# Kernel optimization log

Hardware: AMD Instinct MI355X
Metric: run time of the kernel (lower is better)

Reference implementation:

```python
import jax, jax.numpy as jnp
import numpy as np
from jax import lax

FEAT_STRIDE = 16
SCALES = (8, 16, 32)
RATIOS = (0.5, 1.0, 2.0)
PRE_NMS = 6000
POST_NMS = 300
NMS_THRESH = 0.7
MIN_SIZE = 16.0


def _base_anchors():
    base = 16.0
    cx = cy = base / 2.0
    anchors = []
    for r in RATIOS:
        for s in SCALES:
            h = base * s * np.sqrt(r)
            w = base * s * np.sqrt(1.0 / r)
            anchors.append([cx - w / 2, cy - h / 2, cx + w / 2, cy + h / 2])
    return np.asarray(anchors, np.float32)  # [A,4] (x1,y1,x2,y2)


def _shifted_anchors(h, w):
    base = _base_anchors()
    sy = np.arange(h, dtype=np.float32) * FEAT_STRIDE
    sx = np.arange(w, dtype=np.float32) * FEAT_STRIDE
    yy, xx = np.meshgrid(sy, sx, indexing='ij')  # h-major then w, matching NHWC permute
    shifts = np.stack([xx, yy, xx, yy], axis=-1).reshape(-1, 1, 4)
    return (shifts + base[None]).reshape(-1, 4).astype(np.float32)  # [h*w*A,4]


def _conv(x, w, b, pad):
    y = lax.conv_general_dilated(x, w, (1, 1), [(pad, pad), (pad, pad)],
                                 dimension_numbers=('NCHW', 'OIHW', 'NCHW'))
    return y + b[None, :, None, None]


def _iou(box, boxes):
    lt = jnp.maximum(box[:2], boxes[:, :2])
    rb = jnp.minimum(box[2:], boxes[:, 2:])
    wh = jnp.maximum(rb - lt, 0.0)
    inter = wh[:, 0] * wh[:, 1]
    a1 = (box[2] - box[0]) * (box[3] - box[1])
    a2 = (boxes[:, 2] - boxes[:, 0]) * (boxes[:, 3] - boxes[:, 1])
    return inter / (a1 + a2 - inter + 1e-9)


def _nms_proposals(boxes, scores):
    # boxes [K,4], scores [K] -> [POST_NMS,4]
    ws = boxes[:, 2] - boxes[:, 0]
    hs = boxes[:, 3] - boxes[:, 1]
    scores = jnp.where((ws >= MIN_SIZE) & (hs >= MIN_SIZE), scores, -jnp.inf)
    top_s, idx = lax.top_k(scores, PRE_NMS)
    b = boxes[idx]

    def body(i, st):
        keep, s = st
        j = jnp.argmax(s).astype(jnp.int32)
        keep = keep.at[i].set(j)
        sup = _iou(b[j], b) >= NMS_THRESH  # suppresses j itself too (iou=1)
        s = jnp.where(sup, -jnp.inf, s)
        return keep, s

    keep, _ = lax.fori_loop(0, POST_NMS, body,
                            (jnp.zeros((POST_NMS,), jnp.int32), top_s))
    return b[keep]


def setup_inputs() -> dict:
    key = jax.random.key(0)
    ks = jax.random.split(key, 5)
    n, c, h, w = 8, 512, 50, 64
    A = len(SCALES) * len(RATIOS)
    x = jax.random.normal(ks[0], (n, c, h, w), jnp.float32)
    w1 = jax.random.normal(ks[1], (512, 512, 3, 3), jnp.float32) * 0.02
    b1 = jnp.zeros((512,), jnp.float32)
    w_cls = jax.random.normal(ks[2], (A * 2, 512, 1, 1), jnp.float32) * 0.02
    b_cls = jnp.zeros((A * 2,), jnp.float32)
    w_bbox = jax.random.normal(ks[3], (A * 4, 512, 1, 1), jnp.float32) * 0.005
    b_bbox = jnp.zeros((A * 4,), jnp.float32)
    return {'x': x, 'w1': w1, 'b1': b1, 'w_cls': w_cls, 'b_cls': b_cls,
            'w_bbox': w_bbox, 'b_bbox': b_bbox}


def reference(x, w1, b1, w_cls, b_cls, w_bbox, b_bbox):
    n, _, h, w = x.shape
    A = len(SCALES) * len(RATIOS)
    img_h, img_w = h * FEAT_STRIDE, w * FEAT_STRIDE
    anchors = jnp.asarray(_shifted_anchors(h, w))  # [h*w*A,4]

    feat = jax.nn.relu(_conv(x, w1, b1, 1))
    cls = _conv(feat, w_cls, b_cls, 0).transpose(0, 2, 3, 1).reshape(n, h, w, A, 2)
    fg = jax.nn.softmax(cls, axis=-1)[..., 1].reshape(n, -1)  # [n, h*w*A]
    deltas = _conv(feat, w_bbox, b_bbox, 0).transpose(0, 2, 3, 1).reshape(n, -1, 4)

    # decode deltas against anchors
    aw = anchors[:, 2] - anchors[:, 0]
    ah = anchors[:, 3] - anchors[:, 1]
    acx = anchors[:, 0] + 0.5 * aw
    acy = anchors[:, 1] + 0.5 * ah
    cx = deltas[..., 0] * aw + acx
    cy = deltas[..., 1] * ah + acy
    pw = jnp.exp(deltas[..., 2]) * aw
    ph = jnp.exp(deltas[..., 3]) * ah
    boxes = jnp.stack([cx - 0.5 * pw, cy - 0.5 * ph,
                       cx + 0.5 * pw, cy + 0.5 * ph], axis=-1)  # [n,K,4]
    hi = jnp.asarray([img_w, img_h, img_w, img_h], jnp.float32)
    boxes = jnp.clip(boxes, 0.0, hi)

    rois = jax.vmap(_nms_proposals)(boxes, fg)  # [n,POST_NMS,4]
    roi_indices = jnp.repeat(jnp.arange(n, dtype=jnp.int32), POST_NMS)
    return rois.reshape(-1, 4), roi_indices
```

## Files before the change

kernel.cpp:

```cpp
#include <hip/hip_runtime.h>
#include <math.h>

#define NIMG 8
#define CIN  512
#define HF   50
#define WF   64
#define HW   3200
#define NA   9
#define KPER 28800
#define PRE  6000
#define POST 300

#define WHT_ELEMS  32768

#define NW    94
#define NCAP  6016
#define NTRI  4465

#define XTROWS 52
#define XTCOLS 66
#define XT_ELEMS ((size_t)NIMG * XTROWS * XTCOLS * CIN)
#define XT_BYTES (XT_ELEMS * 2)

#define WPK_ELEMS ((size_t)2 * 4 * 9 * 16 * 4096)
#define WPK_HALF  (4 * 9 * 16 * 4096)

#define SCALE_X 256.0f
#define SCALE_W 16384.0f
#define INV_SCALE (1.0f / 4194304.0f)

#define PB_XT   1600
#define PB_HALO 64
#define PB_WPK  288
#define PB_PH   16
#define PB_TOT  (PB_XT + PB_HALO + PB_WPK + PB_PH)

#define HALO_VPI 14848
#define HALO_TOT (NIMG * HALO_VPI)

typedef _Float16 f16x8 __attribute__((ext_vector_type(8)));
typedef float f32x4  __attribute__((ext_vector_type(4)));
typedef unsigned short u16x8 __attribute__((ext_vector_type(8)));
typedef unsigned long long u64;

__constant__ float BASEA[9][4] = {
  {-82.509667991878083f, -37.254833995939042f,  98.509667991878083f,  53.254833995939042f},
  {-173.01933598375617f, -82.509667991878083f, 189.01933598375617f,   98.509667991878083f},
  {-354.03867196751233f, -173.01933598375617f, 370.03867196751233f,  189.01933598375617f},
  { -56.0f,  -56.0f,  72.0f,  72.0f},
  {-120.0f, -120.0f, 136.0f, 136.0f},
  {-248.0f, -248.0f, 264.0f, 264.0f},
  {-37.254833995939042f, -82.509667991878083f,  53.254833995939042f,  98.509667991878083f},
  {-82.509667991878083f, -173.01933598375617f,  98.509667991878083f, 189.01933598375617f},
  {-173.01933598375617f, -354.03867196751233f, 189.01933598375617f,  370.03867196751233f},
};

__device__ __forceinline__ unsigned int ordf(float f) {
  unsigned int u = __float_as_uint(f);
  return (u & 0x80000000u) ? ~u : (u | 0x80000000u);
}

__device__ __forceinline__ unsigned short f2h(float f) {
  union { _Float16 h; unsigned short u; } cv;
  cv.h = (_Float16)f;
  return cv.u;
}
__device__ __forceinline__ float h2f(unsigned short u) {
  union { _Float16 h; unsigned short u; } cv;
  cv.u = u;
  return (float)cv.h;
}

__global__ __launch_bounds__(256) void k_prep_all(
    const float4* __restrict__ x4,
    const float* __restrict__ w1,
    const float* __restrict__ wc, const float* __restrict__ bc,
    const float* __restrict__ wb, const float* __restrict__ bb,
    unsigned short* __restrict__ xh, unsigned short* __restrict__ xl,
    unsigned short* __restrict__ wpk,
    float* __restrict__ WHT2, float* __restrict__ bh) {
  __shared__ float tile[128][65];
  const int blk = blockIdx.x;
  const int t = threadIdx.x;

  if (blk < PB_XT) {
    const int cic = blk & 3;
    const int rest = blk >> 2;
    const int hrow = rest % 50;
    const int n = rest / 50;
#pragma unroll
    for (int jj = 0; jj < 8; ++jj) {
      const int e = t + 256 * jj;
      const int row = e >> 4, c4 = e & 15;
      const float4 v = x4[(((size_t)(n * CIN + cic * 128 + row) * HF + hrow) << 4) + c4];
      tile[row][c4 * 4 + 0] = v.x;
      tile[row][c4 * 4 + 1] = v.y;
      tile[row][c4 * 4 + 2] = v.z;
      tile[row][c4 * 4 + 3] = v.w;
    }
    __syncthreads();
#pragma unroll
    for (int jj = 0; jj < 4; ++jj) {
      const int e = t + 256 * jj;
      const int w = e >> 4, c8 = e & 15;
      const size_t base = ((size_t)((n * XTROWS + (hrow + 1)) * XTCOLS) + (w + 1)) * CIN
                          + cic * 128 + c8 * 8;
      u16x8 hv, lv;
#pragma unroll
      for (int u = 0; u < 8; ++u) {
        const float g = tile[c8 * 8 + u][w] * SCALE_X;
        const unsigned short hh = f2h(g);
        hv[u] = (short)hh;
        lv[u] = (short)f2h(g - h2f(hh));
      }
      *reinterpret_cast<u16x8*>(xh + base) = hv;
      *reinterpret_cast<u16x8*>(xl + base) = lv;
    }
  } else if (blk < PB_XT + PB_HALO) {
    const u16x8 z = {0, 0, 0, 0, 0, 0, 0, 0};
    const int tid = (blk - PB_XT) * 256 + t;
    for (int v = tid; v < HALO_TOT; v += PB_HALO * 256) {
      const int n = v / HALO_VPI;
      const int r = v - n * HALO_VPI;
      int row, col, v8;
      if (r < 8448) {
        row = (r < 4224) ? 0 : 51;
        const int r2 = (r < 4224) ? r : r - 4224;
        col = r2 >> 6;
        v8 = r2 & 63;
      } else {
        const int q = r - 8448;
        row = 1 + (q >> 7);
        const int rr = q & 127;
        col = (rr >= 64) ? 65 : 0;
        v8 = rr & 63;
      }
      const size_t off = ((size_t)((n * XTROWS + row) * XTCOLS) + col) * CIN + v8 * 8;
      *reinterpret_cast<u16x8*>(xh + off) = z;
      *reinterpret_cast<u16x8*>(xl + off) = z;
    }
  } else if (blk < PB_XT + PB_HALO + PB_WPK) {
    const int tot = (int)WPK_ELEMS;
    const int tid = (blk - PB_XT - PB_HALO) * 256 + t;
    for (int idx = tid; idx < tot; idx += PB_WPK * 256) {
      const int i = idx & 4095;
      int rest = idx >> 12;
      const int ks = rest & 15; rest >>= 4;
      const int tap = rest % 9; rest /= 9;
      const int cob = rest & 3;
      const int sp = rest >> 2;
      const int col = i >> 5;
      const int slotp = (i >> 3) & 3;
      const int j = i & 7;
      const int s = slotp ^ ((col >> 1) & 3);
      const int ci = ks * 32 + s * 8 + j;
      const int co = cob * 128 + col;
      const float g = w1[((size_t)co * CIN + ci) * 9 + tap] * SCALE_W;
      const unsigned short hh = f2h(g);
      wpk[idx] = sp ? f2h(g - h2f(hh)) : hh;
    }
  } else {
    const int TOT = WHT_ELEMS + 64;
    const int tid = (blk - PB_XT - PB_HALO - PB_WPK) * 256 + t;
    for (int idx = tid; idx < TOT; idx += PB_PH * 256) {
      if (idx < WHT_ELEMS) {
        int r = idx & 3;
        int o = (idx >> 2) & 63;
        int c = (idx >> 8) * 4 + r;
        float v = 0.0f;
        if (o < 18) v = wc[(size_t)o * CIN + c];
        else if (o < 54) v = wb[(size_t)(o - 18) * CIN + c];
        WHT2[idx] = v;
      } else {
        int o = idx - WHT_ELEMS;
        float v = 0.0f;
        if (o < 18) v = bc[o];
        else if (o < 54) v = bb[o - 18];
        bh[o] = v;
      }
    }
  }
}

#define GLDS(gp, lp) __builtin_amdgcn_global_load_lds( \
    (const __attribute__((address_space(1))) unsigned int*)(gp), \
    (__attribute__((address_space(3))) unsigned int*)(lp), 16, 0, 0)

__global__ __launch_bounds__(256, 2) void k_convmfma(
    const unsigned short* __restrict__ xh,
    const unsigned short* __restrict__ xl,
    const unsigned short* __restrict__ wpk,
    const float* __restrict__ b1,
    float* __restrict__ feat) {
  __shared__ unsigned short lds[2][4][4096];

  const int raw = blockIdx.x;
  const int xcd = raw & 7;
  const int idx = raw >> 3;
  const int cob = xcd >> 1;
  const int pb  = (xcd & 1) * 100 + idx;

  const int n   = pb / 25;
  const int h0  = (pb - n * 25) * 2;
  const int t   = threadIdx.x;
  const int wid = t >> 6;
  const int l   = t & 63;
  const int wm  = wid >> 1;
  const int wn  = wid & 1;

  const int colp = l >> 2;
  const int sB = (((l & 3) ^ ((l >> 3) & 3)) << 3);
  const unsigned short* xsrc = (wid == 3) ? xl : xh;
  const size_t wA_base = (size_t)(wid & 1) * WPK_HALF;

  const int fr = l & 15;
  const int fq = l >> 4;
  const int slotr = ((fq ^ ((fr >> 1) & 3)) << 4);

  f32x4 acc[4][4] = {};

  auto stage = [&](int sbuf, int ti) {
    const int ks  = ti / 9;
    const int tap = ti - ks * 9;
    if (wid < 2) {
      const unsigned short* gp = wpk + wA_base
          + ((size_t)((cob * 9 + tap) * 16 + ks) << 12) + l * 8;
      unsigned short* lp = &lds[sbuf][wid][0];
#pragma unroll
      for (int q = 0; q < 8; ++q)
        GLDS(gp + q * 512, lp + q * 512);
    } else {
      const int ky = (tap * 11) >> 5;
      const int kx = tap - ky * 3;
      const size_t ebase = ((size_t)((n * XTROWS + h0 + ky) * XTCOLS + kx + colp) << 9)
                           + ks * 32 + sB;
      unsigned short* lp = &lds[sbuf][wid][0];
#pragma unroll
      for (int q = 0; q < 8; ++q)
        GLDS(xsrc + ebase + ((size_t)(((q >> 2) * XTCOLS + (q & 3) * 16)) << 9),
             lp + q * 512);
    }
  };

  stage(0, 0);
  __syncthreads();

  int buf = 0;
  for (int ti = 0; ti < 144; ++ti) {
    if (ti < 143) stage(buf ^ 1, ti + 1);

    f16x8 ah[4], al[4], bhf[4], blf[4];
#pragma unroll
    for (int mi = 0; mi < 4; ++mi) {
      const int off = (((wm << 6) + (mi << 4) + fr) << 6) + slotr;
      ah[mi] = *(const f16x8*)((const char*)&lds[buf][0][0] + off);
      al[mi] = *(const f16x8*)((const char*)&lds[buf][1][0] + off);
    }
#pragma unroll
    for (int ni = 0; ni < 4; ++ni) {
      const int off = (((wn << 6) + (ni << 4) + fr) << 6) + slotr;
      bhf[ni] = *(const f16x8*)((const char*)&lds[buf][2][0] + off);
      blf[ni] = *(const f16x8*)((const char*)&lds[buf][3][0] + off);
    }
#pragma unroll
    for (int mi = 0; mi < 4; ++mi)
#pragma unroll
      for (int ni = 0; ni < 4; ++ni) {
        acc[mi][ni] = __builtin_amdgcn_mfma_f32_16x16x32_f16(ah[mi], bhf[ni], acc[mi][ni], 0, 0, 0);
        acc[mi][ni] = __builtin_amdgcn_mfma_f32_16x16x32_f16(ah[mi], blf[ni], acc[mi][ni], 0, 0, 0);
        acc[mi][ni] = __builtin_amdgcn_mfma_f32_16x16x32_f16(al[mi], bhf[ni], acc[mi][ni], 0, 0, 0);
      }
    __syncthreads();
    buf ^= 1;
  }

  const int h = h0 + wn;
#pragma unroll
  for (int mi = 0; mi < 4; ++mi) {
    const int co = (cob << 7) + (wm << 6) + (mi << 4) + (fq << 2);
    const float4 bias = *(const float4*)&b1[co];
#pragma unroll
    for (int ni = 0; ni < 4; ++ni) {
      const int w = (ni << 4) + fr;
      float4 v;
      v.x = fmaxf(fmaf(acc[mi][ni][0], INV_SCALE, bias.x), 0.0f);
      v.y = fmaxf(fmaf(acc[mi][ni][1], INV_SCALE, bias.y), 0.0f);
      v.z = fmaxf(fmaf(acc[mi][ni][2], INV_SCALE, bias.z), 0.0f);
      v.w = fmaxf(fmaf(acc[mi][ni][3], INV_SCALE, bias.w), 0.0f);
      *(float4*)(feat + (((size_t)n * HW + h * WF + w) << 9) + co) = v;
    }
  }
}

__global__ __launch_bounds__(256) void k_head(const float* __restrict__ feat,
                                              const float* __restrict__ WHT2,
                                              const float* __restrict__ bh,
                                              float* __restrict__ scores,
                                              float4* __restrict__ boxes) {
  __shared__ float fsh[16][512];
  __shared__ float vsh[16][64];
  const int t = threadIdx.x;
  const int wvid = t >> 6;
  const int o = t & 63;
  const int pos0 = blockIdx.x * 16;

  for (int i = t; i < 16 * 512; i += 256)
    fsh[i >> 9][i & 511] = feat[((size_t)pos0 << 9) + i];
  __syncthreads();

  {
    const int p0 = wvid * 4;
    float a0 = 0.f, a1 = 0.f, a2 = 0.f, a3 = 0.f;
    const float4* wp = reinterpret_cast<const float4*>(WHT2);
    const float4* f0 = reinterpret_cast<const float4*>(&fsh[p0 + 0][0]);
    const float4* f1 = reinterpret_cast<const float4*>(&fsh[p0 + 1][0]);
    const float4* f2 = reinterpret_cast<const float4*>(&fsh[p0 + 2][0]);
    const float4* f3 = reinterpret_cast<const float4*>(&fsh[p0 + 3][0]);
#pragma unroll 4
    for (int c4 = 0; c4 < 128; ++c4) {
      float4 w4 = wp[c4 * 64 + o];
      float4 v;
      v = f0[c4];
      a0 = fmaf(w4.x, v.x, a0); a0 = fmaf(w4.y, v.y, a0);
      a0 = fmaf(w4.z, v.z, a0); a0 = fmaf(w4.w, v.w, a0);
      v = f1[c4];
      a1 = fmaf(w4.x, v.x, a1); a1 = fmaf(w4.y, v.y, a1);
      a1 = fmaf(w4.z, v.z, a1); a1 = fmaf(w4.w, v.w, a1);
      v = f2[c4];
      a2 = fmaf(w4.x, v.x, a2); a2 = fmaf(w4.y, v.y, a2);
      a2 = fmaf(w4.z, v.z, a2); a2 = fmaf(w4.w, v.w, a2);
      v = f3[c4];
      a3 = fmaf(w4.x, v.x, a3); a3 = fmaf(w4.y, v.y, a3);
      a3 = fmaf(w4.z, v.z, a3); a3 = fmaf(w4.w, v.w, a3);
    }
    float bv = bh[o];
    vsh[p0 + 0][o] = a0 + bv;
    vsh[p0 + 1][o] = a1 + bv;
    vsh[p0 + 2][o] = a2 + bv;
    vsh[p0 + 3][o] = a3 + bv;
  }
  __syncthreads();

  if (t < 144) {
    const int p2 = t / 9, a = t % 9;
    const int pos = pos0 + p2;
    const int n = pos / HW;
    const int r = pos - n * HW;
    const int ph = r >> 6;
    const int pw = r & 63;

    float l0 = vsh[p2][a * 2];
    float l1 = vsh[p2][a * 2 + 1];
    float m  = fmaxf(l0, l1);
    float e0 = (float)exp((double)__fsub_rn(l0, m));
    float e1 = (float)exp((double)__fsub_rn(l1, m));
    float fg = __fdiv_rn(e1, __fadd_rn(e0, e1));

    float d0 = vsh[p2][18 + a * 4 + 0];
    float d1 = vsh[p2][18 + a * 4 + 1];
    float d2 = vsh[p2][18 + a * 4 + 2];
    float d3 = vsh[p2][18 + a * 4 + 3];

    float sx = (float)(pw * 16);
    float sy = (float)(ph * 16);
    float ax1 = __fadd_rn(BASEA[a][0], sx);
    float ay1 = __fadd_rn(BASEA[a][1], sy);
    float ax2 = __fadd_rn(BASEA[a][2], sx);
    float ay2 = __fadd_rn(BASEA[a][3], sy);
    float aw = __fsub_rn(ax2, ax1);
    float ah = __fsub_rn(ay2, ay1);
    float acx = __fadd_rn(ax1, __fmul_rn(0.5f, aw));
    float acy = __fadd_rn(ay1, __fmul_rn(0.5f, ah));
    float cx = __fadd_rn(__fmul_rn(d0, aw), acx);
    float cy = __fadd_rn(__fmul_rn(d1, ah), acy);
    float pwd = __fmul_rn((float)exp((double)d2), aw);
    float phd = __fmul_rn((float)exp((double)d3), ah);
    float x1 = __fsub_rn(cx, __fmul_rn(0.5f, pwd));
    float y1 = __fsub_rn(cy, __fmul_rn(0.5f, phd));
    float x2 = __fadd_rn(cx, __fmul_rn(0.5f, pwd));
    float y2 = __fadd_rn(cy, __fmul_rn(0.5f, phd));
    x1 = fminf(fmaxf(x1, 0.0f), 1024.0f);
    x2 = fminf(fmaxf(x2, 0.0f), 1024.0f);
    y1 = fminf(fmaxf(y1, 0.0f), 800.0f);
    y2 = fminf(fmaxf(y2, 0.0f), 800.0f);
    float wsz = __fsub_rn(x2, x1);
    float hsz = __fsub_rn(y2, y1);
    float sc = (wsz >= 16.0f && hsz >= 16.0f) ? fg : -__builtin_huge_valf();

    const int idx = n * KPER + r * NA + a;
    scores[idx] = sc;
    boxes[idx] = make_float4(x1, y1, x2, y2);
  }
}

__global__ __launch_bounds__(1024) void k_select(const float* __restrict__ scores,
                                                 const float4* __restrict__ boxes,
                                                 float4* __restrict__ sbox,
                                                 u64* __restrict__ valid) {
  __shared__ u64 sk[8192];
  __shared__ unsigned int whist[16][264];
  __shared__ unsigned int histT[256];
  __shared__ unsigned int sh_selB, sh_ngt, sh_binc, sh_num;
  const int n = blockIdx.x;
  const int t = threadIdx.x;
  const int wv = t >> 6;
  const float* sc = scores + (size_t)n * KPER;

  for (int e = t; e < 8192; e += 1024) sk[e] = 0ull;

  unsigned int prefix = 0, prefMask = 0, ngt = 0, neq = 0;
  for (int shift = 24; shift >= 0; shift -= 8) {
    for (int e = t; e < 16 * 264; e += 1024) (&whist[0][0])[e] = 0u;
    __syncthreads();
    for (int i = t; i < KPER; i += 1024) {
      unsigned int u = ordf(sc[i]);
      if ((u & prefMask) == prefix) atomicAdd(&whist[wv][(u >> shift) & 255], 1u);
    }
    __syncthreads();
    if (t < 256) {
      unsigned int s = 0;
#pragma unroll
      for (int w = 0; w < 16; ++w) s += whist[w][t];
      histT[t] = s;
    }
    __syncthreads();
    if (t == 0) {
      unsigned int cnt = ngt;
      for (int b = 255; b >= 0; --b) {
        unsigned int c = histT[b];
        if (cnt + c >= (unsigned)PRE) { sh_selB = (unsigned)b; sh_ngt = cnt; sh_binc = c; break; }
        cnt += c;
      }
    }
    __syncthreads();
    prefix |= (sh_selB << shift);
    prefMask |= (0xFFu << shift);
    ngt = sh_ngt;
    neq = sh_binc;
    __syncthreads();
  }
  const unsigned int T = prefix;
  const unsigned int needed = (unsigned)PRE - ngt;
  unsigned int J = 0xFFFFFFFFu;
  if (needed < neq) {
    if (t < 256) histT[t] = 0;
    __syncthreads();
    for (int i = t; i < KPER; i += 1024)
      if (ordf(sc[i]) == T) atomicAdd(&histT[i >> 7], 1u);
    __syncthreads();
    if (t == 0) {
      unsigned int cnt = 0;
      for (int b = 0; b < 256; ++b) {
        unsigned int c = histT[b];
        if (cnt + c >= needed) { sh_selB = (unsigned)b; sh_ngt = needed - cnt; break; }
        cnt += c;
      }
    }
    __syncthreads();
    const unsigned int selH = sh_selB;
    const unsigned int needLow = sh_ngt;
    __syncthreads();
    if (t < 128) histT[t] = 0;
    __syncthreads();
    for (int i = t; i < KPER; i += 1024)
      if (ordf(sc[i]) == T && ((unsigned)(i >> 7)) == selH) atomicAdd(&histT[i & 127], 1u);
    __syncthreads();
    if (t == 0) {
      unsigned int cnt = 0;
      for (int b = 0; b < 128; ++b) {
        unsigned int c = histT[b];
        if (cnt + c >= needLow) { sh_selB = (selH << 7) | (unsigned)b; break; }
        cnt += c;
      }
    }
    __syncthreads();
    J = sh_selB;
  }

  if (t == 0) sh_num = 0;
  __syncthreads();
  for (int i = t; i < KPER; i += 1024) {
    unsigned int u = ordf(sc[i]);
    bool in = (u > T) || (u == T && (unsigned)i <= J);
    if (in) {
      unsigned int p = atomicAdd(&sh_num, 1u);
      sk[p] = (((u64)u) << 32) | (u64)(~(unsigned int)i);
    }
  }
  __syncthreads();

  for (int k = 2; k <= 8192; k <<= 1) {
    for (int j = k >> 1; j > 0; j >>= 1) {
      for (int p = t; p < 4096; p += 1024) {
        const int i = ((p & ~(j - 1)) << 1) | (p & (j - 1));
        const int ip = i | j;
        u64 a = sk[i], b = sk[ip];
        const bool desc = ((i & k) == 0);
        if ((a < b) == desc) { sk[i] = b; sk[ip] = a; }
      }
      __syncthreads();
    }
  }

  for (int e = t; e < NCAP; e += 1024) {
    float4 bx = make_float4(0.f, 0.f, 0.f, 0.f);
    if (e < PRE) {
      unsigned idx = ~(unsigned)(sk[e] & 0xFFFFFFFFull);
      bx = boxes[(size_t)n * KPER + idx];
    }
    sbox[(size_t)n * NCAP + e] = bx;
  }
  if (t < 128) {
    u64 w = 0;
    if (t < NW) {
      for (int b = 0; b < 64; ++b) {
        int e = t * 64 + b;
        if (e < PRE && ((sk[e] >> 32) > 0x007FFFFFull)) w |= 1ull << b;
      }
    }
    valid[n * 128 + t] = w;
  }
}

__global__ __launch_bounds__(64) void k_mask(const float4* __restrict__ sbox,
                                             u64* __restrict__ mask) {
  const int p = blockIdx.x;
  const int n = blockIdx.y;
  int ib = (int)((189.0 - sqrt(35721.0 - 8.0 * (double)p)) * 0.5);
  while (94 * (ib + 1) - (ib * (ib + 1)) / 2 <= p) ++ib;
  while (94 * ib - ((ib - 1) * ib) / 2 > p) --ib;
  const int jb = ib + (p - (94 * ib - ((ib - 1) * ib) / 2));

  const int r = threadIdx.x;
  const int i = ib * 64 + r;
  __shared__ float4 jbox[64];
  jbox[r] = sbox[(size_t)n * NCAP + jb * 64 + r];
  __syncthreads();
  const float4 pbx = sbox[(size_t)n * NCAP + i];
  const float pa = __fmul_rn(__fsub_rn(pbx.z, pbx.x), __fsub_rn(pbx.w, pbx.y));
  u64 word = 0;
#pragma unroll 8
  for (int b = 0; b < 64; ++b) {
    const float4 q = jbox[b];
    float ltx = fmaxf(pbx.x, q.x);
    float lty = fmaxf(pbx.y, q.y);
    float rbx = fminf(pbx.z, q.z);
    float rby = fminf(pbx.w, q.w);
    float wv = fmaxf(__fsub_rn(rbx, ltx), 0.0f);
    float hv = fmaxf(__fsub_rn(rby, lty), 0.0f);
    float inter = __fmul_rn(wv, hv);
    float a2 = __fmul_rn(__fsub_rn(q.z, q.x), __fsub_rn(q.w, q.y));
    float denom = __fadd_rn(__fsub_rn(__fadd_rn(pa, a2), inter), 1e-9f);
    float iou = __fdiv_rn(inter, denom);
    if (iou >= 0.7f) word |= (1ull << b);
  }
  mask[((size_t)(n * NCAP) + i) * NW + jb] = word;
}

__global__ __launch_bounds__(64) void k_scan(const u64* __restrict__ mask,
                                             const u64* __restrict__ valid,
                                             const float4* __restrict__ sbox,
                                             float* __restrict__ out) {
  const int n = blockIdx.x;
  const int lane = threadIdx.x;
  u64 s0 = 0, s1 = 0;
  const u64 v0 = valid[n * 128 + 2 * lane];
  const u64 v1 = valid[n * 128 + 2 * lane + 1];
  const u64* mrow = mask + (size_t)n * NCAP * NW;
  __shared__ int keep_list[POST];
  int kept = 0;

  ulonglong2 cur[16], nxt[16];
#pragma unroll
  for (int r = 0; r < 16; ++r)
    cur[r] = ((const ulonglong2*)(mrow + (size_t)r * NW))[lane];

  for (int g = 0; g < PRE / 16; ++g) {
    if (kept >= POST) break;
    if (g < PRE / 16 - 1) {
#pragma unroll
      for (int r = 0; r < 16; ++r)
        nxt[r] = ((const ulonglong2*)(mrow + (size_t)((g + 1) * 16 + r) * NW))[lane];
    }
#pragma unroll
    for (int r = 0; r < 16; ++r) {
      if (kept < POST) {
        const int i = g * 16 + r;
        const int w = i >> 6;
        const u64 avail = (w & 1) ? (v1 & ~s1) : (v0 & ~s0);
        const unsigned h32 = (unsigned)(avail >> (i & 32));
        const unsigned wrd = __shfl(h32, w >> 1, 64);
        if ((wrd >> (i & 31)) & 1u) {
          if (lane == 0) keep_list[kept] = i;
          ++kept;
          s0 |= cur[r].x;
          s1 |= cur[r].y;
        }
      }
    }
#pragma unroll
    for (int r = 0; r < 16; ++r) cur[r] = nxt[r];
  }
  __syncthreads();

  for (int it = lane; it < POST; it += 64) {
    const int cand = (it < kept) ? keep_list[it] : 0;
    const float4 b = sbox[(size_t)n * NCAP + cand];
    float* orow = out + ((size_t)n * POST + it) * 4;
    orow[0] = b.x; orow[1] = b.y; orow[2] = b.z; orow[3] = b.w;
    out[(size_t)NIMG * POST * 4 + (size_t)n * POST + it] = (float)n;
  }
}

extern "C" void kernel_launch(void* const* d_in, const int* in_sizes, int n_in,
                              void* d_out, int out_size, void* d_ws, size_t ws_size,
                              hipStream_t stream) {
  const float* x    = (const float*)d_in[0];
  const float* w1   = (const float*)d_in[1];
  const float* b1   = (const float*)d_in[2];
  const float* wcls = (const float*)d_in[3];
  const float* bcls = (const float*)d_in[4];
  const float* wbb  = (const float*)d_in[5];
  const float* bbb  = (const float*)d_in[6];
  float* out = (float*)d_out;

  char* ws = (char*)d_ws;
  size_t off = 0;
  float* feat = (float*)(ws + off);               off += (size_t)NIMG * HW * CIN * 4;
  float* scores = (float*)(ws + off);             off += (size_t)NIMG * KPER * 4;
  float4* boxes = (float4*)(ws + off);            off += (size_t)NIMG * KPER * 16;
  float4* sbox = (float4*)(ws + off);             off += (size_t)NIMG * NCAP * 16;
  u64* valid = (u64*)(ws + off);                  off += (size_t)NIMG * 128 * 8;
  u64* mask = (u64*)(ws + off);                   off += (size_t)NIMG * NCAP * NW * 8;
  float* WHT2 = (float*)(ws + off);               off += (size_t)WHT_ELEMS * 4;
  float* bh   = (float*)(ws + off);               off += 256;
  unsigned short* xTh = (unsigned short*)(ws + off); off += XT_BYTES;
  unsigned short* xTl = (unsigned short*)(ws + off); off += XT_BYTES;
  unsigned short* wpk = (unsigned short*)(ws + off); off += WPK_ELEMS * 2;

  k_prep_all<<<PB_TOT, 256, 0, stream>>>((const float4*)x, w1, wcls, bcls, wbb, bbb,
                                         xTh, xTl, wpk, WHT2, bh);
  k_convmfma<<<800, 256, 0, stream>>>(xTh, xTl, wpk, b1, feat);
  k_head<<<(NIMG * HW) / 16, 256, 0, stream>>>(feat, WHT2, bh, scores, boxes);
  k_select<<<NIMG, 1024, 0, stream>>>(scores, boxes, sbox, valid);
  k_mask<<<dim3(NTRI, NIMG), 64, 0, stream>>>(sbox, mask);
  k_scan<<<NIMG, 64, 0, stream>>>(mask, valid, sbox, out);
}
```

Baseline: 760.5 us.

## Jump NMS scan to next surviving candidate with speculative row prefetch

The serial NMS scan no longer walks all 6000 candidates in groups of 16. It finds the next unsuppressed candidate with a ballot plus count-trailing-zeros search, and prefetches the mask rows of the next four predicted survivors. The prefetch is refilled whenever a suppression invalidates the prediction. Separately, the score reads in k_select and the feature staging in k_head now use float4 vector loads. The aim is to cut the latency-bound per-candidate iteration of the single-wave scan, at the cost of extra ballot/shuffle work per kept box and occasional wasted prefetches.

Result: slower. 878.6 us (+15.5%).

```diff
diff --git a/kernel.cpp b/kernel.cpp
--- a/kernel.cpp
+++ b/kernel.cpp
@@ -16,6 +16,7 @@
 #define NW    94
 #define NCAP  6016
 #define NTRI  4465
+#define CINF  0x7FFFFFFF
 
 #define XTROWS 52
 #define XTCOLS 66
@@ -304,8 +305,12 @@
   const int o = t & 63;
   const int pos0 = blockIdx.x * 16;
 
-  for (int i = t; i < 16 * 512; i += 256)
-    fsh[i >> 9][i & 511] = feat[((size_t)pos0 << 9) + i];
+  {
+    const float4* fsrc = reinterpret_cast<const float4*>(feat + ((size_t)pos0 << 9));
+    float4* fdst = reinterpret_cast<float4*>(&fsh[0][0]);
+#pragma unroll
+    for (int i = 0; i < 8; ++i) fdst[t + 256 * i] = fsrc[t + 256 * i];
+  }
   __syncthreads();
 
   {
@@ -405,6 +410,7 @@
   const int t = threadIdx.x;
   const int wv = t >> 6;
   const float* sc = scores + (size_t)n * KPER;
+  const float4* sc4 = reinterpret_cast<const float4*>(sc);
 
   for (int e = t; e < 8192; e += 1024) sk[e] = 0ull;
 
@@ -412,9 +418,13 @@
   for (int shift = 24; shift >= 0; shift -= 8) {
     for (int e = t; e < 16 * 264; e += 1024) (&whist[0][0])[e] = 0u;
     __syncthreads();
-    for (int i = t; i < KPER; i += 1024) {
-      unsigned int u = ordf(sc[i]);
-      if ((u & prefMask) == prefix) atomicAdd(&whist[wv][(u >> shift) & 255], 1u);
+    for (int i4 = t; i4 < KPER / 4; i4 += 1024) {
+      const float4 v = sc4[i4];
+      unsigned int u;
+      u = ordf(v.x); if ((u & prefMask) == prefix) atomicAdd(&whist[wv][(u >> shift) & 255], 1u);
+      u = ordf(v.y); if ((u & prefMask) == prefix) atomicAdd(&whist[wv][(u >> shift) & 255], 1u);
+      u = ordf(v.z); if ((u & prefMask) == prefix) atomicAdd(&whist[wv][(u >> shift) & 255], 1u);
+      u = ordf(v.w); if ((u & prefMask) == prefix) atomicAdd(&whist[wv][(u >> shift) & 255], 1u);
     }
     __syncthreads();
     if (t < 256) {
@@ -479,12 +489,18 @@
 
   if (t == 0) sh_num = 0;
   __syncthreads();
-  for (int i = t; i < KPER; i += 1024) {
-    unsigned int u = ordf(sc[i]);
-    bool in = (u > T) || (u == T && (unsigned)i <= J);
-    if (in) {
-      unsigned int p = atomicAdd(&sh_num, 1u);
-      sk[p] = (((u64)u) << 32) | (u64)(~(unsigned int)i);
+  for (int i4 = t; i4 < KPER / 4; i4 += 1024) {
+    const float4 v = sc4[i4];
+    const float vv[4] = {v.x, v.y, v.z, v.w};
+#pragma unroll
+    for (int c = 0; c < 4; ++c) {
+      const int i = i4 * 4 + c;
+      unsigned int u = ordf(vv[c]);
+      bool in = (u > T) || (u == T && (unsigned)i <= J);
+      if (in) {
+        unsigned int p = atomicAdd(&sh_num, 1u);
+        sk[p] = (((u64)u) << 32) | (u64)(~(unsigned int)i);
+      }
     }
   }
   __syncthreads();
@@ -566,40 +582,64 @@
   u64 s0 = 0, s1 = 0;
   const u64 v0 = valid[n * 128 + 2 * lane];
   const u64 v1 = valid[n * 128 + 2 * lane + 1];
-  const u64* mrow = mask + (size_t)n * NCAP * NW;
+  const u64* mbase = mask + (size_t)n * NCAP * NW;
   __shared__ int keep_list[POST];
+
+  auto clr_le = [](u64 w, int local) -> u64 {
+    if (local < 0) return w;
+    if (local >= 63) return 0ull;
+    return w & ~((2ull << local) - 1);
+  };
+  auto find_next = [&](int from) -> int {
+    u64 m0 = clr_le(v0 & ~s0, from - lane * 128);
+    u64 m1 = clr_le(v1 & ~s1, from - lane * 128 - 64);
+    int loc = CINF;
+    if (m0) loc = lane * 128 + (int)__builtin_ctzll(m0);
+    else if (m1) loc = lane * 128 + 64 + (int)__builtin_ctzll(m1);
+    u64 nz = __ballot(loc != CINF);
+    int r = CINF;
+    if (nz) r = __shfl(loc, (int)__builtin_ctzll(nz), 64);
+    return r;
+  };
+  auto rowld = [&](int c) -> ulonglong2 {
+    ulonglong2 q; q.x = 0ull; q.y = 0ull;
+    const int cc = (c < NCAP) ? c : 0;
+    if (lane < 47)
+      q = reinterpret_cast<const ulonglong2*>(mbase + (size_t)cc * NW)[lane];
+    return q;
+  };
+
+  int c0 = find_next(-1);
+  int c1 = find_next(c0);
+  int c2 = find_next(c1);
+  int c3 = find_next(c2);
+  ulonglong2 pf0 = rowld(c0);
+  ulonglong2 pf1 = rowld(c1);
+  ulonglong2 pf2 = rowld(c2);
+  ulonglong2 pf3 = rowld(c3);
+
   int kept = 0;
-
-  ulonglong2 cur[16], nxt[16];
-#pragma unroll
-  for (int r = 0; r < 16; ++r)
-    cur[r] = ((const ulonglong2*)(mrow + (size_t)r * NW))[lane];
-
-  for (int g = 0; g < PRE / 16; ++g) {
-    if (kept >= POST) break;
-    if (g < PRE / 16 - 1) {
-#pragma unroll
-      for (int r = 0; r < 16; ++r)
-        nxt[r] = ((const ulonglong2*)(mrow + (size_t)((g + 1) * 16 + r) * NW))[lane];
-    }
-#pragma unroll
-    for (int r = 0; r < 16; ++r) {
-      if (kept < POST) {
-        const int i = g * 16 + r;
-        const int w = i >> 6;
-        const u64 avail = (w & 1) ? (v1 & ~s1) : (v0 & ~s0);
-        const unsigned h32 = (unsigned)(avail >> (i & 32));
-        const unsigned wrd = __shfl(h32, w >> 1, 64);
-        if ((wrd >> (i & 31)) & 1u) {
-          if (lane == 0) keep_list[kept] = i;
-          ++kept;
-          s0 |= cur[r].x;
-          s1 |= cur[r].y;
-        }
-      }
-    }
-#pragma unroll
-    for (int r = 0; r < 16; ++r) cur[r] = nxt[r];
+  while (kept < POST && c0 != CINF) {
+    if (lane == 0) keep_list[kept] = c0;
+    ++kept;
+    s0 |= pf0.x;
+    s1 |= pf0.y;
+    const int nx = find_next(c0);
+    if (nx == c1) {
+      c0 = c1; c1 = c2; c2 = c3;
+      pf0 = pf1; pf1 = pf2; pf2 = pf3;
+      c3 = find_next(c2);
+      pf3 = rowld(c3);
+    } else {
+      c0 = nx;
+      c1 = find_next(c0);
+      c2 = find_next(c1);
+      c3 = find_next(c2);
+      pf0 = rowld(c0);
+      pf1 = rowld(c1);
+      pf2 = rowld(c2);
+      pf3 = rowld(c3);
+    }
   }
   __syncthreads();
 
```

## Vectorize score and feature loads, deepen NMS scan mask prefetch to two groups

Applied to the files above, without the earlier changes.

The head kernel now loads its feature tile into shared memory as float4, and the top-k select kernel reads scores as float4 in both its histogram and compaction passes, which cuts the number of load instructions. The serial NMS scan kernel switches from a one-group-ahead register prefetch of mask rows to a three-buffer rotation that prefetches two groups ahead, to hide global memory latency in the single-wave bitmask scan. This raises register pressure in the scan kernel (48 ulonglong2 per lane) and adds copy overhead on each rotation.

Result: no change. 747.8 us (-1.7%).

```diff
diff --git a/kernel.cpp b/kernel.cpp
--- a/kernel.cpp
+++ b/kernel.cpp
@@ -304,8 +304,12 @@
   const int o = t & 63;
   const int pos0 = blockIdx.x * 16;
 
-  for (int i = t; i < 16 * 512; i += 256)
-    fsh[i >> 9][i & 511] = feat[((size_t)pos0 << 9) + i];
+  {
+    const float4* fsrc = reinterpret_cast<const float4*>(feat + ((size_t)pos0 << 9));
+    float4* fdst = reinterpret_cast<float4*>(&fsh[0][0]);
+#pragma unroll
+    for (int i = 0; i < 8; ++i) fdst[t + 256 * i] = fsrc[t + 256 * i];
+  }
   __syncthreads();
 
   {
@@ -405,6 +409,7 @@
   const int t = threadIdx.x;
   const int wv = t >> 6;
   const float* sc = scores + (size_t)n * KPER;
+  const float4* sc4 = reinterpret_cast<const float4*>(sc);
 
   for (int e = t; e < 8192; e += 1024) sk[e] = 0ull;
 
@@ -412,9 +417,13 @@
   for (int shift = 24; shift >= 0; shift -= 8) {
     for (int e = t; e < 16 * 264; e += 1024) (&whist[0][0])[e] = 0u;
     __syncthreads();
-    for (int i = t; i < KPER; i += 1024) {
-      unsigned int u = ordf(sc[i]);
-      if ((u & prefMask) == prefix) atomicAdd(&whist[wv][(u >> shift) & 255], 1u);
+    for (int i4 = t; i4 < KPER / 4; i4 += 1024) {
+      const float4 v = sc4[i4];
+      unsigned int u;
+      u = ordf(v.x); if ((u & prefMask) == prefix) atomicAdd(&whist[wv][(u >> shift) & 255], 1u);
+      u = ordf(v.y); if ((u & prefMask) == prefix) atomicAdd(&whist[wv][(u >> shift) & 255], 1u);
+      u = ordf(v.z); if ((u & prefMask) == prefix) atomicAdd(&whist[wv][(u >> shift) & 255], 1u);
+      u = ordf(v.w); if ((u & prefMask) == prefix) atomicAdd(&whist[wv][(u >> shift) & 255], 1u);
     }
     __syncthreads();
     if (t < 256) {
@@ -479,12 +488,18 @@
 
   if (t == 0) sh_num = 0;
   __syncthreads();
-  for (int i = t; i < KPER; i += 1024) {
-    unsigned int u = ordf(sc[i]);
-    bool in = (u > T) || (u == T && (unsigned)i <= J);
-    if (in) {
-      unsigned int p = atomicAdd(&sh_num, 1u);
-      sk[p] = (((u64)u) << 32) | (u64)(~(unsigned int)i);
+  for (int i4 = t; i4 < KPER / 4; i4 += 1024) {
+    const float4 v = sc4[i4];
+    const float vv[4] = {v.x, v.y, v.z, v.w};
+#pragma unroll
+    for (int c = 0; c < 4; ++c) {
+      const int i = i4 * 4 + c;
+      unsigned int u = ordf(vv[c]);
+      bool in = (u > T) || (u == T && (unsigned)i <= J);
+      if (in) {
+        unsigned int p = atomicAdd(&sh_num, 1u);
+        sk[p] = (((u64)u) << 32) | (u64)(~(unsigned int)i);
+      }
     }
   }
   __syncthreads();
@@ -570,17 +585,21 @@
   __shared__ int keep_list[POST];
   int kept = 0;
 
-  ulonglong2 cur[16], nxt[16];
+  const int NG = PRE / 16;
+  ulonglong2 c0[16], c1[16], c2[16];
 #pragma unroll
   for (int r = 0; r < 16; ++r)
-    cur[r] = ((const ulonglong2*)(mrow + (size_t)r * NW))[lane];
-
-  for (int g = 0; g < PRE / 16; ++g) {
+    c0[r] = ((const ulonglong2*)(mrow + (size_t)r * NW))[lane];
+#pragma unroll
+  for (int r = 0; r < 16; ++r)
+    c1[r] = ((const ulonglong2*)(mrow + (size_t)(16 + r) * NW))[lane];
+
+  for (int g = 0; g < NG; ++g) {
     if (kept >= POST) break;
-    if (g < PRE / 16 - 1) {
+    if (g + 2 < NG) {
 #pragma unroll
       for (int r = 0; r < 16; ++r)
-        nxt[r] = ((const ulonglong2*)(mrow + (size_t)((g + 1) * 16 + r) * NW))[lane];
+        c2[r] = ((const ulonglong2*)(mrow + (size_t)((g + 2) * 16 + r) * NW))[lane];
     }
 #pragma unroll
     for (int r = 0; r < 16; ++r) {
@@ -593,13 +612,13 @@
         if ((wrd >> (i & 31)) & 1u) {
           if (lane == 0) keep_list[kept] = i;
           ++kept;
-          s0 |= cur[r].x;
-          s1 |= cur[r].y;
+          s0 |= c0[r].x;
+          s1 |= c0[r].y;
         }
       }
     }
 #pragma unroll
-    for (int r = 0; r < 16; ++r) cur[r] = nxt[r];
+    for (int r = 0; r < 16; ++r) { c0[r] = c1[r]; c1[r] = c2[r]; }
   }
   __syncthreads();
 
```
